# Optimization experiments

Hardware: AMD Instinct MI355X
Metric: run time of the kernel (lower is better)

## Reference

```python
import jax, jax.numpy as jnp
import numpy as np


def _knn_idx(query, ref, k):
    # query [B,Q,F], ref [B,M,F] -> indices [B,Q,k] of k nearest refs (L2)
    d2 = (jnp.sum(query * query, -1)[..., None]
          - 2.0 * jnp.einsum('bqf,bmf->bqm', query, ref)
          + jnp.sum(ref * ref, -1)[:, None, :])
    _, idx = jax.lax.top_k(-d2, k)
    return idx


def _gather(pts, idx):
    # pts [B,M,F], idx [B,Q,k] -> [B,Q,k,F]
    return jax.vmap(lambda p, i: p[i])(pts, idx)


def _mlp(h, W1, b1, W2, b2):
    # pointwise 1x1-conv MLP: Conv1d(k=1) == per-point matmul
    return jax.nn.relu(h @ W1 + b1) @ W2 + b2


def setup_inputs() -> dict:
    key = jax.random.key(0)
    ks = jax.random.split(key, 12)
    B, N, S1, S2 = 8, 16384, 512, 128

    def p(k, shape, fan):
        return jax.random.normal(k, shape, jnp.float32) / np.float32(np.sqrt(fan))

    return {
        'x': jax.random.normal(ks[0], (B, N, 3), jnp.float32),
        'sample_idx1': jnp.sort(jax.random.randint(ks[1], (S1,), 0, N)),
        'sample_idx2': jnp.sort(jax.random.randint(ks[2], (S2,), 0, S1)),
        'sa1_W1': p(ks[3], (3, 64), 3), 'sa1_b1': jnp.zeros((64,), jnp.float32),
        'sa1_W2': p(ks[4], (64, 64), 64), 'sa1_b2': jnp.zeros((64,), jnp.float32),
        'sa2_W1': p(ks[5], (64, 128), 64), 'sa2_b1': jnp.zeros((128,), jnp.float32),
        'sa2_W2': p(ks[6], (128, 128), 128), 'sa2_b2': jnp.zeros((128,), jnp.float32),
        'fp1_W1': p(ks[7], (192, 64), 192), 'fp1_b1': jnp.zeros((64,), jnp.float32),
        'fp1_W2': p(ks[8], (64, 64), 64), 'fp1_b2': jnp.zeros((64,), jnp.float32),
        'fp2_W1': p(ks[9], (67, 32), 67), 'fp2_b1': jnp.zeros((32,), jnp.float32),
        'fp2_W2': p(ks[10], (32, 32), 32), 'fp2_b2': jnp.zeros((32,), jnp.float32),
        'fc_W': p(ks[11], (32, 2), 32), 'fc_b': jnp.zeros((2,), jnp.float32),
    }


def reference(x, sample_idx1, sample_idx2,
              sa1_W1, sa1_b1, sa1_W2, sa1_b2,
              sa2_W1, sa2_b1, sa2_W2, sa2_b2,
              fp1_W1, fp1_b1, fp1_W2, fp1_b2,
              fp2_W1, fp2_b1, fp2_W2, fp2_b2,
              fc_W, fc_b):
    G = 32  # group_points
    # --- SetAbstraction 1 (KNN grouping in xyz space) ---
    samp1 = x[:, sample_idx1]                                  # [B,S1,3]
    g1 = _gather(x, _knn_idx(samp1, x, G))                     # [B,S1,G,3]
    feat1 = jnp.max(_mlp(g1, sa1_W1, sa1_b1, sa1_W2, sa1_b2), axis=2)   # [B,S1,64]
    # --- SetAbstraction 2 (point cloud = SA1 features, as in source) ---
    samp2 = feat1[:, sample_idx2]                              # [B,S2,64]
    g2 = _gather(feat1, _knn_idx(samp2, feat1, G))             # [B,S2,G,64]
    feat2 = jnp.max(_mlp(g2, sa2_W1, sa2_b1, sa2_W2, sa2_b2), axis=2)   # [B,S2,128]
    coords2 = samp1[:, sample_idx2]                            # [B,S2,3]
    # --- FeaturePropagation 1: interpolate feat2 onto the S1 points (3-NN mean) ---
    interp1 = jnp.mean(_gather(feat2, _knn_idx(samp1, coords2, 3)), axis=2)  # [B,S1,128]
    h1 = _mlp(jnp.concatenate([feat1, interp1], -1), fp1_W1, fp1_b1, fp1_W2, fp1_b2)  # [B,S1,64]
    # --- FeaturePropagation 2: interpolate onto all N points ---
    interp2 = jnp.mean(_gather(h1, _knn_idx(x, samp1, 3)), axis=2)           # [B,N,64]
    h2 = _mlp(jnp.concatenate([x, interp2], -1), fp2_W1, fp2_b1, fp2_W2, fp2_b2)      # [B,N,32]
    return jax.nn.sigmoid(h2 @ fc_W + fc_b)                    # [B,N,2]
```

## Files before the change

### kernel.cpp

```cpp
#include <hip/hip_runtime.h>
#include <hip/hip_bf16.h>

#define NB   8
#define NPTS 16384
#define NS1  512
#define NS2  128
#define KNN  32
#define FINF 3.402823466e+38f
#define NINF_BITS ((int)0xFF800000)

__device__ __forceinline__ void topk32f(float key, int idx, int lane,
                                        float& lkey, int& lidx, float& tau,
                                        unsigned long long mask) {
  const bool is16 = (lane == 16);
  while (mask) {
    const int src = (int)(__ffsll((long long)mask) - 1);
    mask &= mask - 1;
    const float ck = __int_as_float(
        __builtin_amdgcn_readlane(__float_as_int(key), src));
    if (ck < tau) {
      const int ci = __builtin_amdgcn_readlane(idx, src);
      const int upk0 = __builtin_amdgcn_update_dpp(
          NINF_BITS, __float_as_int(lkey), 0x111, 0xf, 0xf, false);
      const int upi0 = __builtin_amdgcn_update_dpp(
          0, lidx, 0x111, 0xf, 0xf, false);
      const int pk = __builtin_amdgcn_readlane(__float_as_int(lkey), 15);
      const int pi = __builtin_amdgcn_readlane(lidx, 15);
      const float up  = __int_as_float(is16 ? pk : upk0);
      const int   upi = is16 ? pi : upi0;
      const bool keep  = (lkey <= ck);
      const bool useup = (up > ck);
      const float nk = keep ? lkey : (useup ? up : ck);
      const int   ni = keep ? lidx : (useup ? upi : ci);
      if (lane < 32) { lkey = nk; lidx = ni; }
      tau = __int_as_float(__builtin_amdgcn_readlane(__float_as_int(lkey), 31));
    }
  }
}

__device__ __forceinline__ void merge3(float& d0, int& j0, float& d1, int& j1,
                                       float& d2, int& j2, int xm) {
  float e0 = __shfl_xor(d0, xm), e1 = __shfl_xor(d1, xm), e2 = __shfl_xor(d2, xm);
  int   f0 = __shfl_xor(j0, xm), f1 = __shfl_xor(j1, xm), f2 = __shfl_xor(j2, xm);
  float a0 = d0, a1 = d1, a2 = d2;
  int   b0 = j0, b1 = j1, b2 = j2;
  float od0, od1, od2; int oj0, oj1, oj2;
  #pragma unroll
  for (int r = 0; r < 3; ++r) {
    bool ta = (a0 < e0) || (a0 == e0 && b0 < f0);
    float sd = ta ? a0 : e0; int sj = ta ? b0 : f0;
    a0 = ta ? a1 : a0;  b0 = ta ? b1 : b0;
    a1 = ta ? a2 : a1;  b1 = ta ? b2 : b1;
    a2 = ta ? FINF : a2;
    e0 = ta ? e0 : e1;  f0 = ta ? f0 : f1;
    e1 = ta ? e1 : e2;  f1 = ta ? f1 : f2;
    e2 = ta ? e2 : FINF;
    if (r == 0) { od0 = sd; oj0 = sj; }
    else if (r == 1) { od1 = sd; oj1 = sj; }
    else { od2 = sd; oj2 = sj; }
  }
  d0 = od0; j0 = oj0; d1 = od1; j1 = oj1; d2 = od2; j2 = oj2;
}

extern "C" __global__ void __launch_bounds__(256)
prep_kernel(const float* __restrict__ x, float4* __restrict__ xr) {
  const int i = blockIdx.x * 256 + threadIdx.x;
  const float rx = x[i*3+0], ry = x[i*3+1], rz = x[i*3+2];
  xr[i] = make_float4(rx, ry, rz, rx*rx + ry*ry + rz*rz);
}

#define PROCF(rr, jbase)                                                      \
  {                                                                           \
    const float d = (Q.w - 2.0f*(Q.x*rr.x + Q.y*rr.y + Q.z*rr.z)) + rr.w;     \
    const unsigned long long mask = __ballot(d < tau);                        \
    if (mask) topk32f(d, (jbase) + lane, lane, lkey, lidx, tau, mask);        \
  }

extern "C" __global__ void __launch_bounds__(256)
knn1_kernel(const float4* __restrict__ xr, const int* __restrict__ sidx1,
            int* __restrict__ idx1) {
  const int w = threadIdx.x >> 6, lane = threadIdx.x & 63;
  const int gq = blockIdx.x * 4 + w;
  const int b = gq >> 9, q = gq & (NS1 - 1);
  const float4* xb = xr + (size_t)b * NPTS;
  const float4 Q = xb[sidx1[q]];
  float lkey = FINF, tau = FINF;
  int lidx = 0;
  float4 r0 = xb[0*64+lane], r1 = xb[1*64+lane], r2 = xb[2*64+lane], r3 = xb[3*64+lane];
  float4 r4 = xb[4*64+lane], r5 = xb[5*64+lane], r6 = xb[6*64+lane], r7 = xb[7*64+lane];
  for (int t = 0; t < 256; t += 8) {
    PROCF(r0, (t+0)*64);  r0 = xb[((t+ 8)&255)*64 + lane];
    PROCF(r1, (t+1)*64);  r1 = xb[((t+ 9)&255)*64 + lane];
    PROCF(r2, (t+2)*64);  r2 = xb[((t+10)&255)*64 + lane];
    PROCF(r3, (t+3)*64);  r3 = xb[((t+11)&255)*64 + lane];
    PROCF(r4, (t+4)*64);  r4 = xb[((t+12)&255)*64 + lane];
    PROCF(r5, (t+5)*64);  r5 = xb[((t+13)&255)*64 + lane];
    PROCF(r6, (t+6)*64);  r6 = xb[((t+14)&255)*64 + lane];
    PROCF(r7, (t+7)*64);  r7 = xb[((t+15)&255)*64 + lane];
  }
  if (lane < 32) idx1[gq*KNN + lane] = lidx;
}

extern "C" __global__ void __launch_bounds__(256)
mlp1_kernel(const float* __restrict__ x, const int* __restrict__ sidx1,
            const int* __restrict__ idx1,
            const float* __restrict__ W1, const float* __restrict__ b1,
            const float* __restrict__ W2, const float* __restrict__ b2,
            float* __restrict__ feat1, float* __restrict__ rr1,
            float* __restrict__ samp1) {
  __shared__ float P[32][3];
  __shared__ float H[32][64];
  __shared__ float PM[4][64];
  const int tid = threadIdx.x;
  const int gq = blockIdx.x;
  const int b = gq >> 9, q = gq & (NS1-1);
  const float* xb = x + (size_t)b * NPTS * 3;
  const int* nb = idx1 + gq * KNN;
  if (tid < 96) { int n = tid/3, d = tid - n*3; P[n][d] = xb[nb[n]*3 + d]; }
  __syncthreads();
  #pragma unroll
  for (int i = 0; i < 8; ++i) {
    int e = tid + 256*i, n = e >> 6, c = e & 63;
    float h = b1[c] + P[n][0]*W1[c] + P[n][1]*W1[64+c] + P[n][2]*W1[128+c];
    H[n][c] = fmaxf(h, 0.0f);
  }
  __syncthreads();
  const int g = tid >> 6, c = tid & 63;
  float acc[8];
  #pragma unroll
  for (int k = 0; k < 8; ++k) acc[k] = 0.0f;
  for (int j = 0; j < 64; j += 4) {
    float w0 = W2[j*64+c], w1 = W2[(j+1)*64+c], w2 = W2[(j+2)*64+c], w3 = W2[(j+3)*64+c];
    #pragma unroll
    for (int k = 0; k < 8; ++k) {
      float4 h4 = *(const float4*)&H[g*8+k][j];
      acc[k] = fmaf(h4.w, w3, fmaf(h4.z, w2, fmaf(h4.y, w1, fmaf(h4.x, w0, acc[k]))));
    }
  }
  float m = acc[0];
  #pragma unroll
  for (int k = 1; k < 8; ++k) m = fmaxf(m, acc[k]);
  PM[g][c] = m;
  __syncthreads();
  if (tid < 64) {
    float v = fmaxf(fmaxf(PM[0][tid], PM[1][tid]), fmaxf(PM[2][tid], PM[3][tid])) + b2[tid];
    feat1[(size_t)gq*64 + tid] = v;
    float s = v*v;
    #pragma unroll
    for (int off = 32; off; off >>= 1) s += __shfl_xor(s, off);
    if (tid == 0) rr1[gq] = s;
  } else if (tid < 67) {
    int d = tid - 64;
    samp1[(size_t)gq*3 + d] = xb[sidx1[q]*3 + d];
  }
}

extern "C" __global__ void __launch_bounds__(256)
knn2mlp2_kernel(const float* __restrict__ feat1, const float* __restrict__ rr1,
                const int* __restrict__ sidx2,
                const float* __restrict__ W1, const float* __restrict__ b1,
                const float* __restrict__ W2, const float* __restrict__ b2,
                float* __restrict__ feat2) {
  __shared__ float qrow[64];
  __shared__ float SK[4][32];
  __shared__ int   SI[4][32];
  __shared__ int   NBs[32];
  __shared__ float Gm[32][64];
  __shared__ float H[32][128];
  __shared__ float PM[2][128];
  const int tid = threadIdx.x, w = tid >> 6, lane = tid & 63;
  const int gq = blockIdx.x;
  const int b = gq >> 7, q = gq & (NS2-1);
  const float* f1b = feat1 + (size_t)b * NS1 * 64;
  const float* rrb = rr1 + b * NS1;
  const int sq = sidx2[q];
  if (tid < 64) qrow[tid] = f1b[sq*64 + tid];
  __syncthreads();
  const float qq = rrb[sq];
  float lkey = FINF, tau = FINF;
  int lidx = 0;
  #pragma unroll
  for (int t = 0; t < 2; ++t) {
    const int j = w*128 + t*64 + lane;
    const float* rrow = f1b + j*64;
    float dot = 0.0f;
    #pragma unroll
    for (int f = 0; f < 64; f += 4) {
      float4 r4 = *(const float4*)(rrow + f);
      dot = fmaf(qrow[f+3], r4.w, fmaf(qrow[f+2], r4.z,
            fmaf(qrow[f+1], r4.y, fmaf(qrow[f+0], r4.x, dot))));
    }
    const float d = (qq - 2.0f*dot) + rrb[j];
    const unsigned long long mask = __ballot(d < tau);
    if (mask) topk32f(d, j, lane, lkey, lidx, tau, mask);
  }
  if (lane < 32) { SK[w][lane] = lkey; SI[w][lane] = lidx; }
  __syncthreads();
  if (w == 0) {
    #pragma unroll
    for (int ww = 1; ww < 4; ++ww) {
      const float mk = (lane < 32) ? SK[ww][lane] : FINF;
      const int   mi = (lane < 32) ? SI[ww][lane] : 0;
      const unsigned long long mmask = __ballot(mk < tau);
      if (mmask) topk32f(mk, mi, lane, lkey, lidx, tau, mmask);
    }
    if (lane < 32) NBs[lane] = lidx;
  }
  __syncthreads();
  #pragma unroll
  for (int i = 0; i < 8; ++i) {
    int e = tid + 256*i, n = e >> 6, f = e & 63;
    Gm[n][f] = f1b[NBs[n]*64 + f];
  }
  __syncthreads();
  #pragma unroll
  for (int i = 0; i < 16; ++i) {
    int e = tid + 256*i, n = e >> 7, c = e & 127;
    float h = b1[c];
    for (int f = 0; f < 64; f += 4) {
      float4 g4 = *(const float4*)&Gm[n][f];
      h = fmaf(g4.x, W1[f*128+c], h);
      h = fmaf(g4.y, W1[(f+1)*128+c], h);
      h = fmaf(g4.z, W1[(f+2)*128+c], h);
      h = fmaf(g4.w, W1[(f+3)*128+c], h);
    }
    H[n][c] = fmaxf(h, 0.0f);
  }
  __syncthreads();
  const int g = tid >> 7, c = tid & 127;
  float acc[16];
  #pragma unroll
  for (int k = 0; k < 16; ++k) acc[k] = 0.0f;
  for (int j = 0; j < 128; j += 4) {
    float w0 = W2[j*128+c], w1 = W2[(j+1)*128+c], w2 = W2[(j+2)*128+c], w3 = W2[(j+3)*128+c];
    #pragma unroll
    for (int k = 0; k < 16; ++k) {
      float4 h4 = *(const float4*)&H[g*16+k][j];
      acc[k] = fmaf(h4.w, w3, fmaf(h4.z, w2, fmaf(h4.y, w1, fmaf(h4.x, w0, acc[k]))));
    }
  }
  float m = acc[0];
  #pragma unroll
  for (int k = 1; k < 16; ++k) m = fmaxf(m, acc[k]);
  PM[g][c] = m;
  __syncthreads();
  if (tid < 128) feat2[(size_t)gq*128 + tid] = fmaxf(PM[0][tid], PM[1][tid]) + b2[tid];
}

extern "C" __global__ void __launch_bounds__(256)
fp1_kernel(const float* __restrict__ samp1, const int* __restrict__ sidx2,
           const float* __restrict__ feat1, const float* __restrict__ feat2,
           const float* __restrict__ W1, const float* __restrict__ b1,
           const float* __restrict__ W2, const float* __restrict__ b2,
           float* __restrict__ h1) {
  __shared__ float interp[4][128];
  __shared__ float hbuf[4][64];
  const int w = threadIdx.x >> 6, lane = threadIdx.x & 63;
  const int gq = blockIdx.x*4 + w;
  const int b = gq >> 9, q = gq & (NS1-1);
  const float* s1b = samp1 + (size_t)b * NS1 * 3;
  const float qx = s1b[q*3+0], qy = s1b[q*3+1], qz = s1b[q*3+2];
  const float qq = qx*qx + qy*qy + qz*qz;
  float d0, d1; int j0i, j1i;
  {
    const int rs = sidx2[lane];
    const float rx = s1b[rs*3+0], ry = s1b[rs*3+1], rz = s1b[rs*3+2];
    d0 = (qq - 2.0f*(qx*rx+qy*ry+qz*rz)) + (rx*rx+ry*ry+rz*rz);
    j0i = lane;
  }
  {
    const int j = lane + 64;
    const int rs = sidx2[j];
    const float rx = s1b[rs*3+0], ry = s1b[rs*3+1], rz = s1b[rs*3+2];
    d1 = (qq - 2.0f*(qx*rx+qy*ry+qz*rz)) + (rx*rx+ry*ry+rz*rz);
    j1i = j;
  }
  if (d1 < d0) { float td = d0; d0 = d1; d1 = td; int tj = j0i; j0i = j1i; j1i = tj; }
  float dA = d0, dB = d1, dC = FINF;
  int   jA = j0i, jB = j1i, jC = 0;
  merge3(dA, jA, dB, jB, dC, jC, 1);
  merge3(dA, jA, dB, jB, dC, jC, 2);
  merge3(dA, jA, dB, jB, dC, jC, 4);
  merge3(dA, jA, dB, jB, dC, jC, 8);
  merge3(dA, jA, dB, jB, dC, jC, 16);
  merge3(dA, jA, dB, jB, dC, jC, 32);
  const int r0 = jA, r1 = jB, r2 = jC;
  const float* f2b = feat2 + (size_t)b * NS2 * 128;
  interp[w][lane] =
      (f2b[r0*128+lane] + f2b[r1*128+lane] + f2b[r2*128+lane]) * (1.0f/3.0f);
  interp[w][lane+64] =
      (f2b[r0*128+64+lane] + f2b[r1*128+64+lane] + f2b[r2*128+64+lane]) * (1.0f/3.0f);
  __syncthreads();
  const float* f1row = feat1 + (size_t)gq * 64;
  float h = b1[lane];
  for (int f = 0; f < 64; ++f)  h = fmaf(f1row[f], W1[f*64+lane], h);
  for (int f = 0; f < 128; ++f) h = fmaf(interp[w][f], W1[(64+f)*64+lane], h);
  hbuf[w][lane] = fmaxf(h, 0.0f);
  __syncthreads();
  float o = b2[lane];
  for (int f = 0; f < 64; ++f) o = fmaf(hbuf[w][f], W2[f*64+lane], o);
  h1[(size_t)gq*64 + lane] = o;
}

extern "C" __global__ void __launch_bounds__(256, 3)
fp2_kernel(const float* __restrict__ x, const float* __restrict__ samp1,
           const float* __restrict__ h1,
           const float* __restrict__ W1, const float* __restrict__ b1,
           const float* __restrict__ W2, const float* __restrict__ b2,
           const float* __restrict__ fcW, const float* __restrict__ fcb,
           float* __restrict__ out) {
  __shared__ float4 RS[NS1];
  __shared__ ushort4 kid[64];
  __shared__ float Xe[64][68];
  __shared__ float W1s[67*32];
  __shared__ float Hs[64][36];
  __shared__ float WcS[64];
  __shared__ float bcS[2];
  const int tid = threadIdx.x;
  const int b = blockIdx.x >> 8;
  const int pbase = (blockIdx.x & 255) * 64;
  const float* xb = x + (size_t)b * NPTS * 3;
  const float* h1b = h1 + (size_t)b * NS1 * 64;
  for (int e = tid; e < NS1; e += 256) {
    const float rx = samp1[((size_t)b*NS1 + e)*3 + 0];
    const float ry = samp1[((size_t)b*NS1 + e)*3 + 1];
    const float rz = samp1[((size_t)b*NS1 + e)*3 + 2];
    RS[e] = make_float4(rx, ry, rz, rx*rx + ry*ry + rz*rz);
  }
  for (int e = tid; e < 67*32; e += 256) W1s[e] = W1[e];
  if (tid < 64) {
    Xe[tid][0] = xb[(pbase+tid)*3+0];
    Xe[tid][1] = xb[(pbase+tid)*3+1];
    Xe[tid][2] = xb[(pbase+tid)*3+2];
  }
  __syncthreads();
  {
    const int pl = tid >> 2, q4 = tid & 3;
    const float qx = Xe[pl][0], qy = Xe[pl][1], qz = Xe[pl][2];
    const float qq = qx*qx + qy*qy + qz*qz;
    float d0 = FINF, d1 = FINF, d2 = FINF;
    int j0 = 0, j1 = 0, j2 = 0;
    const float4* RQ = RS + q4*128;
    #pragma unroll 4
    for (int i = 0; i < 128; ++i) {
      const float4 r = RQ[i];
      const float dot = qx*r.x + qy*r.y + qz*r.z;
      const float d = (qq - 2.0f*dot) + r.w;
      const int j = q4*128 + i;
      const bool c2 = d < d2, c1 = d < d1, c0 = d < d0;
      d2 = c1 ? d1 : (c2 ? d : d2);  j2 = c1 ? j1 : (c2 ? j : j2);
      d1 = c0 ? d0 : (c1 ? d : d1);  j1 = c0 ? j0 : (c1 ? j : j1);
      d0 = c0 ? d : d0;              j0 = c0 ? j : j0;
    }
    merge3(d0, j0, d1, j1, d2, j2, 1);
    merge3(d0, j0, d1, j1, d2, j2, 2);
    if (q4 == 0) {
      ushort4 o;
      o.x = (unsigned short)j0; o.y = (unsigned short)j1;
      o.z = (unsigned short)j2; o.w = 0;
      kid[pl] = o;
    }
  }
  __syncthreads();
  {
    const int sub = tid >> 6, f = tid & 63;
    #pragma unroll 4
    for (int i = 0; i < 16; ++i) {
      const int p = i*4 + sub;
      const ushort4 kk = kid[p];
      const float v = (h1b[(int)kk.x*64 + f] + h1b[(int)kk.y*64 + f] +
                       h1b[(int)kk.z*64 + f]) * (1.0f/3.0f);
      Xe[p][3+f] = v;
    }
  }
  __syncthreads();
  if (tid < 64) {
    const int k = tid >> 1, col = tid & 1;
    float s = 0.0f;
    for (int c = 0; c < 32; ++c) s = fmaf(W2[k*32+c], fcW[c*2+col], s);
    WcS[k*2+col] = s;
  } else if (tid < 66) {
    const int col = tid & 1;
    float s = fcb[col];
    for (int c = 0; c < 32; ++c) s = fmaf(b2[c], fcW[c*2+col], s);
    bcS[col] = s;
  }
  {
    const int p = tid >> 2, c0 = (tid & 3) * 8;
    float acc[8];
    const float4 bb0 = *(const float4*)(b1 + c0);
    const float4 bb1 = *(const float4*)(b1 + c0 + 4);
    acc[0]=bb0.x; acc[1]=bb0.y; acc[2]=bb0.z; acc[3]=bb0.w;
    acc[4]=bb1.x; acc[5]=bb1.y; acc[6]=bb1.z; acc[7]=bb1.w;
    for (int f = 0; f < 67; ++f) {
      const float xv = Xe[p][f];
      const float4 w0 = *(const float4*)&W1s[f*32 + c0];
      const float4 w1 = *(const float4*)&W1s[f*32 + c0 + 4];
      acc[0] = fmaf(xv, w0.x, acc[0]);
      acc[1] = fmaf(xv, w0.y, acc[1]);
      acc[2] = fmaf(xv, w0.z, acc[2]);
      acc[3] = fmaf(xv, w0.w, acc[3]);
      acc[4] = fmaf(xv, w1.x, acc[4]);
      acc[5] = fmaf(xv, w1.y, acc[5]);
      acc[6] = fmaf(xv, w1.z, acc[6]);
      acc[7] = fmaf(xv, w1.w, acc[7]);
    }
    *(float4*)&Hs[p][c0]   = make_float4(fmaxf(acc[0],0.f), fmaxf(acc[1],0.f),
                                         fmaxf(acc[2],0.f), fmaxf(acc[3],0.f));
    *(float4*)&Hs[p][c0+4] = make_float4(fmaxf(acc[4],0.f), fmaxf(acc[5],0.f),
                                         fmaxf(acc[6],0.f), fmaxf(acc[7],0.f));
  }
  __syncthreads();
  if (tid < 128) {
    const int p = tid >> 1, col = tid & 1;
    float s = bcS[col];
    for (int c = 0; c < 32; ++c) s = fmaf(Hs[p][c], WcS[c*2+col], s);
    out[((size_t)b*NPTS + pbase + p)*2 + col] = 1.0f / (1.0f + expf(-s));
  }
}

extern "C" void kernel_launch(void* const* d_in, const int* in_sizes, int n_in,
                              void* d_out, int out_size, void* d_ws, size_t ws_size,
                              hipStream_t stream) {
  const float* x     = (const float*)d_in[0];
  const int*   sidx1 = (const int*)d_in[1];
  const int*   sidx2 = (const int*)d_in[2];
  const float* sa1W1 = (const float*)d_in[3];
  const float* sa1b1 = (const float*)d_in[4];
  const float* sa1W2 = (const float*)d_in[5];
  const float* sa1b2 = (const float*)d_in[6];
  const float* sa2W1 = (const float*)d_in[7];
  const float* sa2b1 = (const float*)d_in[8];
  const float* sa2W2 = (const float*)d_in[9];
  const float* sa2b2 = (const float*)d_in[10];
  const float* fp1W1 = (const float*)d_in[11];
  const float* fp1b1 = (const float*)d_in[12];
  const float* fp1W2 = (const float*)d_in[13];
  const float* fp1b2 = (const float*)d_in[14];
  const float* fp2W1 = (const float*)d_in[15];
  const float* fp2b1 = (const float*)d_in[16];
  const float* fp2W2 = (const float*)d_in[17];
  const float* fp2b2 = (const float*)d_in[18];
  const float* fcW   = (const float*)d_in[19];
  const float* fcb   = (const float*)d_in[20];
  float* out = (float*)d_out;

  char* ws = (char*)d_ws;
  float4* xr   = (float4*)(ws + 0);
  float* feat1 = (float*)(ws + 0);
  float* rr1   = (float*)(ws + 1048576);
  float* samp1 = (float*)(ws + 1064960);
  float* feat2 = (float*)(ws + 1114112);
  float* h1    = (float*)(ws + 1638400);
  int*   idx1  = (int*)  (ws + 2686976);

  hipLaunchKernelGGL(prep_kernel, dim3(512), dim3(256), 0, stream, x, xr);
  hipLaunchKernelGGL(knn1_kernel, dim3(1024), dim3(256), 0, stream,
                     xr, sidx1, idx1);
  hipLaunchKernelGGL(mlp1_kernel, dim3(4096), dim3(256), 0, stream,
                     x, sidx1, idx1, sa1W1, sa1b1, sa1W2, sa1b2,
                     feat1, rr1, samp1);
  hipLaunchKernelGGL(knn2mlp2_kernel, dim3(1024), dim3(256), 0, stream,
                     feat1, rr1, sidx2, sa2W1, sa2b1, sa2W2, sa2b2, feat2);
  hipLaunchKernelGGL(fp1_kernel, dim3(1024), dim3(256), 0, stream,
                     samp1, sidx2, feat1, feat2, fp1W1, fp1b1, fp1W2, fp1b2, h1);
  hipLaunchKernelGGL(fp2_kernel, dim3(2048), dim3(256), 0, stream,
                     x, samp1, h1, fp2W1, fp2b1, fp2W2, fp2b2, fcW, fcb, out);
}
```

Before: 245.1 us.

## Process two KNN queries per wavefront in SA1 top-32 selection

knn1 now assigns two query points to each wavefront: lanes 0-31 hold the sorted top-32 list for query A and lanes 32-63 hold the list for query B. Both queries share every loaded reference point, and their insertions run in one interleaved loop using DPP shifts plus readlane fixups at lanes 16 and 48. The grid is halved to match. The goal is to halve reference-point loads and the number of serial insertion loops per query, at the cost of more work per insertion step and some divergence when one query has more candidates than the other. It also adds a scan variant that computes the index as jbase+src instead of reading it with readlane, used in knn2.

```diff
diff --git a/kernel.cpp b/kernel.cpp
--- a/kernel.cpp
+++ b/kernel.cpp
@@ -9,9 +9,38 @@
 #define FINF 3.402823466e+38f
 #define NINF_BITS ((int)0xFF800000)
 
-__device__ __forceinline__ void topk32f(float key, int idx, int lane,
-                                        float& lkey, int& lidx, float& tau,
-                                        unsigned long long mask) {
+__device__ __forceinline__ void topk32f_scan(float key, int jbase, int lane,
+                                             float& lkey, int& lidx, float& tau,
+                                             unsigned long long mask) {
+  const bool is16 = (lane == 16);
+  while (mask) {
+    const int src = (int)(__ffsll((long long)mask) - 1);
+    mask &= mask - 1;
+    const float ck = __int_as_float(
+        __builtin_amdgcn_readlane(__float_as_int(key), src));
+    if (ck < tau) {
+      const int ci = jbase + src;
+      const int upk0 = __builtin_amdgcn_update_dpp(
+          NINF_BITS, __float_as_int(lkey), 0x111, 0xf, 0xf, false);
+      const int upi0 = __builtin_amdgcn_update_dpp(
+          0, lidx, 0x111, 0xf, 0xf, false);
+      const int pk = __builtin_amdgcn_readlane(__float_as_int(lkey), 15);
+      const int pi = __builtin_amdgcn_readlane(lidx, 15);
+      const float up  = __int_as_float(is16 ? pk : upk0);
+      const int   upi = is16 ? pi : upi0;
+      const bool keep  = (lkey <= ck);
+      const bool useup = (up > ck);
+      const float nk = keep ? lkey : (useup ? up : ck);
+      const int   ni = keep ? lidx : (useup ? upi : ci);
+      if (lane < 32) { lkey = nk; lidx = ni; }
+      tau = __int_as_float(__builtin_amdgcn_readlane(__float_as_int(lkey), 31));
+    }
+  }
+}
+
+__device__ __forceinline__ void topk32f_merge(float key, int idx, int lane,
+                                              float& lkey, int& lidx, float& tau,
+                                              unsigned long long mask) {
   const bool is16 = (lane == 16);
   while (mask) {
     const int src = (int)(__ffsll((long long)mask) - 1);
@@ -69,36 +98,77 @@
   xr[i] = make_float4(rx, ry, rz, rx*rx + ry*ry + rz*rz);
 }
 
-#define PROCF(rr, jbase)                                                      \
+#define PROC2(rr, jbase)                                                      \
   {                                                                           \
-    const float d = (Q.w - 2.0f*(Q.x*rr.x + Q.y*rr.y + Q.z*rr.z)) + rr.w;     \
-    const unsigned long long mask = __ballot(d < tau);                        \
-    if (mask) topk32f(d, (jbase) + lane, lane, lkey, lidx, tau, mask);        \
+    const float dA = (QA.w - 2.0f*(QA.x*rr.x + QA.y*rr.y + QA.z*rr.z)) + rr.w;\
+    const float dB = (QB.w - 2.0f*(QB.x*rr.x + QB.y*rr.y + QB.z*rr.z)) + rr.w;\
+    unsigned long long mA = __ballot(dA < tauA);                              \
+    unsigned long long mB = __ballot(dB < tauB);                              \
+    while (mA | mB) {                                                         \
+      float ckA = FINF, ckB = FINF; int ciA = 0, ciB = 0;                     \
+      bool doA = false, doB = false;                                          \
+      if (mA) {                                                               \
+        const int sA = (int)(__ffsll((long long)mA) - 1); mA &= mA - 1;       \
+        ckA = __int_as_float(__builtin_amdgcn_readlane(__float_as_int(dA), sA)); \
+        ciA = (jbase) + sA;  doA = (ckA < tauA);                              \
+      }                                                                       \
+      if (mB) {                                                               \
+        const int sB = (int)(__ffsll((long long)mB) - 1); mB &= mB - 1;       \
+        ckB = __int_as_float(__builtin_amdgcn_readlane(__float_as_int(dB), sB)); \
+        ciB = (jbase) + sB;  doB = (ckB < tauB);                              \
+      }                                                                       \
+      if (doA | doB) {                                                        \
+        int upk = __builtin_amdgcn_update_dpp(                                \
+            NINF_BITS, __float_as_int(lkey), 0x111, 0xf, 0xf, false);         \
+        int upi = __builtin_amdgcn_update_dpp(0, lidx, 0x111, 0xf, 0xf, false); \
+        const int pk15 = __builtin_amdgcn_readlane(__float_as_int(lkey), 15); \
+        const int pi15 = __builtin_amdgcn_readlane(lidx, 15);                 \
+        const int pk47 = __builtin_amdgcn_readlane(__float_as_int(lkey), 47); \
+        const int pi47 = __builtin_amdgcn_readlane(lidx, 47);                 \
+        if (is16) { upk = pk15; upi = pi15; }                                 \
+        if (is48) { upk = pk47; upi = pi47; }                                 \
+        const float up = __int_as_float(upk);                                 \
+        const float ck = isA ? ckA : ckB;                                     \
+        const int   ci = isA ? ciA : ciB;                                     \
+        const bool commit = isA ? doA : doB;                                  \
+        const bool keep  = (lkey <= ck);                                      \
+        const bool useup = (up > ck);                                         \
+        const float nk = keep ? lkey : (useup ? up : ck);                     \
+        const int   ni = keep ? lidx : (useup ? upi : ci);                    \
+        if (commit) { lkey = nk; lidx = ni; }                                 \
+        tauA = __int_as_float(__builtin_amdgcn_readlane(__float_as_int(lkey), 31)); \
+        tauB = __int_as_float(__builtin_amdgcn_readlane(__float_as_int(lkey), 63)); \
+      }                                                                       \
+    }                                                                         \
   }
 
 extern "C" __global__ void __launch_bounds__(256)
 knn1_kernel(const float4* __restrict__ xr, const int* __restrict__ sidx1,
             int* __restrict__ idx1) {
   const int w = threadIdx.x >> 6, lane = threadIdx.x & 63;
-  const int gq = blockIdx.x * 4 + w;
-  const int b = gq >> 9, q = gq & (NS1 - 1);
+  const int gw = blockIdx.x * 4 + w;
+  const int qA = gw * 2, qB = qA + 1;
+  const int b = qA >> 9;
   const float4* xb = xr + (size_t)b * NPTS;
-  const float4 Q = xb[sidx1[q]];
-  float lkey = FINF, tau = FINF;
+  const float4 QA = xb[sidx1[qA & (NS1-1)]];
+  const float4 QB = xb[sidx1[qB & (NS1-1)]];
+  const bool isA = (lane < 32), is16 = (lane == 16), is48 = (lane == 48);
+  float lkey = FINF, tauA = FINF, tauB = FINF;
   int lidx = 0;
   float4 r0 = xb[0*64+lane], r1 = xb[1*64+lane], r2 = xb[2*64+lane], r3 = xb[3*64+lane];
   float4 r4 = xb[4*64+lane], r5 = xb[5*64+lane], r6 = xb[6*64+lane], r7 = xb[7*64+lane];
   for (int t = 0; t < 256; t += 8) {
-    PROCF(r0, (t+0)*64);  r0 = xb[((t+ 8)&255)*64 + lane];
-    PROCF(r1, (t+1)*64);  r1 = xb[((t+ 9)&255)*64 + lane];
-    PROCF(r2, (t+2)*64);  r2 = xb[((t+10)&255)*64 + lane];
-    PROCF(r3, (t+3)*64);  r3 = xb[((t+11)&255)*64 + lane];
-    PROCF(r4, (t+4)*64);  r4 = xb[((t+12)&255)*64 + lane];
-    PROCF(r5, (t+5)*64);  r5 = xb[((t+13)&255)*64 + lane];
-    PROCF(r6, (t+6)*64);  r6 = xb[((t+14)&255)*64 + lane];
-    PROCF(r7, (t+7)*64);  r7 = xb[((t+15)&255)*64 + lane];
-  }
-  if (lane < 32) idx1[gq*KNN + lane] = lidx;
+    PROC2(r0, (t+0)*64);  r0 = xb[((t+ 8)&255)*64 + lane];
+    PROC2(r1, (t+1)*64);  r1 = xb[((t+ 9)&255)*64 + lane];
+    PROC2(r2, (t+2)*64);  r2 = xb[((t+10)&255)*64 + lane];
+    PROC2(r3, (t+3)*64);  r3 = xb[((t+11)&255)*64 + lane];
+    PROC2(r4, (t+4)*64);  r4 = xb[((t+12)&255)*64 + lane];
+    PROC2(r5, (t+5)*64);  r5 = xb[((t+13)&255)*64 + lane];
+    PROC2(r6, (t+6)*64);  r6 = xb[((t+14)&255)*64 + lane];
+    PROC2(r7, (t+7)*64);  r7 = xb[((t+15)&255)*64 + lane];
+  }
+  if (isA) idx1[qA*KNN + lane] = lidx;
+  else     idx1[qB*KNN + (lane - 32)] = lidx;
 }
 
 extern "C" __global__ void __launch_bounds__(256)
@@ -181,7 +251,8 @@
   int lidx = 0;
   #pragma unroll
   for (int t = 0; t < 2; ++t) {
-    const int j = w*128 + t*64 + lane;
+    const int jb = w*128 + t*64;
+    const int j = jb + lane;
     const float* rrow = f1b + j*64;
     float dot = 0.0f;
     #pragma unroll
@@ -192,7 +263,7 @@
     }
     const float d = (qq - 2.0f*dot) + rrb[j];
     const unsigned long long mask = __ballot(d < tau);
-    if (mask) topk32f(d, j, lane, lkey, lidx, tau, mask);
+    if (mask) topk32f_scan(d, jb, lane, lkey, lidx, tau, mask);
   }
   if (lane < 32) { SK[w][lane] = lkey; SI[w][lane] = lidx; }
   __syncthreads();
@@ -202,7 +273,7 @@
       const float mk = (lane < 32) ? SK[ww][lane] : FINF;
       const int   mi = (lane < 32) ? SI[ww][lane] : 0;
       const unsigned long long mmask = __ballot(mk < tau);
-      if (mmask) topk32f(mk, mi, lane, lkey, lidx, tau, mmask);
+      if (mmask) topk32f_merge(mk, mi, lane, lkey, lidx, tau, mmask);
     }
     if (lane < 32) NBs[lane] = lidx;
   }
@@ -455,7 +526,7 @@
   int*   idx1  = (int*)  (ws + 2686976);
 
   hipLaunchKernelGGL(prep_kernel, dim3(512), dim3(256), 0, stream, x, xr);
-  hipLaunchKernelGGL(knn1_kernel, dim3(1024), dim3(256), 0, stream,
+  hipLaunchKernelGGL(knn1_kernel, dim3(512), dim3(256), 0, stream,
                      xr, sidx1, idx1);
   hipLaunchKernelGGL(mlp1_kernel, dim3(4096), dim3(256), 0, stream,
                      x, sidx1, idx1, sa1W1, sa1b1, sa1W2, sa1b2,
```

Result: slower. 273.9 us (+11.8%).
